# Kernel tuning notes

Hardware: AMD Instinct MI355X
Metric: run time of the kernel (lower is better)

The kernel has to match this reference:

```python
import jax, jax.numpy as jnp
import numpy as np

GRID = (32, 32, 32)
LOWER = jnp.array([0.0, 0.0, 0.0], jnp.float32)
UPPER = jnp.array([1.0, 1.0, 1.0], jnp.float32)
B = 16
N = 131072
C_IN = 1018          # per-point feature channels; +3 offset +3 xyz = 1024 = nn_channels[0]
D_IN = 1024
C_OUT = 128          # nn_channels[-1]
BN_EPS = 1e-5


def setup_inputs() -> dict:
    key = jax.random.key(0)
    ks = jax.random.split(key, 8)
    W1 = jax.random.normal(ks[5], (D_IN, C_OUT), jnp.float32) / np.sqrt(D_IN).astype(np.float32)
    return {
        "xyz": jax.random.uniform(ks[0], (N, 3), jnp.float32),
        "pred_nocs": jax.random.uniform(ks[1], (N, 3), jnp.float32),
        "per_point_features": jax.random.normal(ks[2], (N, C_IN), jnp.float32),
        "pred_confidence": jax.random.uniform(ks[3], (N, 1), jnp.float32),
        "batch_idx": jnp.sort(jax.random.randint(ks[4], (N,), 0, B, dtype=jnp.int32)),
        "batch_size": B,
        "W1": W1,
        "b1": jnp.zeros((C_OUT,), jnp.float32),
        "g1": jnp.ones((C_OUT,), jnp.float32),
        "be1": jnp.zeros((C_OUT,), jnp.float32),
    }


def _batchnorm_train(x, gamma, beta):
    # torch BatchNorm1d in training mode: biased variance over the batch dim
    m = jnp.mean(x, axis=0)
    v = jnp.mean(jnp.square(x - m), axis=0)
    return (x - m) * jax.lax.rsqrt(v + BN_EPS) * gamma + beta


def reference(xyz, pred_nocs, per_point_features, pred_confidence, batch_idx,
              batch_size, W1, b1, g1, be1):
    gs_f = jnp.array(GRID, jnp.float32)
    gs_i = jnp.array(GRID, jnp.int32)
    # VirtualGrid.get_points_grid_idxs: round to nearest cell, clip into grid
    idx_f = jnp.round((pred_nocs - LOWER) / (UPPER - LOWER) * (gs_f - 1.0))
    idx = jnp.clip(idx_f.astype(jnp.int32), 0, gs_i - 1)  # [N,3]
    # VirtualGrid.idxs_to_points
    grid_pts = idx.astype(jnp.float32) / (gs_f - 1.0) * (UPPER - LOWER) + LOWER
    local_offset = pred_nocs - grid_pts
    feats = jnp.concatenate([per_point_features, local_offset, xyz], axis=-1)  # [N,1024]
    # local_nn: Linear -> ReLU -> PointBatchNorm1D
    h = _batchnorm_train(jax.nn.relu(feats @ W1 + b1), g1, be1)  # [N,128]
    # flatten (b,i,j,k) -> flat grid index
    gx, gy, gz = GRID
    flat = ((batch_idx.astype(jnp.int32) * gx + idx[:, 0]) * gy + idx[:, 1]) * gz + idx[:, 2]
    num_grids = batch_size * gx * gy * gz
    ssum = jax.ops.segment_sum(h, flat, num_segments=num_grids)          # [num_grids,128]
    cnt = jax.ops.segment_sum(jnp.ones((h.shape[0], 1), h.dtype), flat, num_segments=num_grids)
    mean = ssum / jnp.maximum(cnt, 1.0)  # empty cells stay 0 (torch_scatter mean)
    # [num_grids, C] -> [B, gx, gy, gz, C] -> [B, C, gx, gy, gz]
    vol = mean.reshape(batch_size, gx, gy, gz, C_OUT).transpose(0, 4, 1, 2, 3)
    return vol
```

## Files before the change

### kernel.cpp

```cpp
#include <hip/hip_runtime.h>

#define NPTS   131072
#define CIN    1018
#define DIN    1024
#define COUT   128
#define BB     16
#define GDIM   32
#define NCELLS (BB*GDIM*GDIM*GDIM)

typedef float          f32x4  __attribute__((ext_vector_type(4)));
typedef __bf16         bf16x8 __attribute__((ext_vector_type(8)));
typedef unsigned short us8    __attribute__((ext_vector_type(8)));

__device__ __forceinline__ unsigned short f2bf(float f) {
    union { float f; unsigned u; } v; v.f = f;
    unsigned r = v.u + 0x7FFFu + ((v.u >> 16) & 1u);
    return (unsigned short)(r >> 16);
}

__global__ __launch_bounds__(256) void k_packW(const float* __restrict__ W1,
                                               unsigned short* __restrict__ pw) {
    const int t  = blockIdx.x * 256 + threadIdx.x;
    const int l  = t & 63;
    const int cb = (t >> 6) & 7;
    const int ks = t >> 9;
    const int col  = cb * 16 + (l & 15);
    const int krow = ks * 32 + ((l >> 4) * 8);
    unsigned short* dst = pw + (size_t)t * 8;
#pragma unroll
    for (int i = 0; i < 8; ++i) dst[i] = f2bf(W1[(size_t)(krow + i) * COUT + col]);
}

__global__ __launch_bounds__(256) void k_prep(const float* __restrict__ xyz,
                                              const float* __restrict__ nocs,
                                              const float* __restrict__ feats,
                                              const int*   __restrict__ bidx,
                                              float* __restrict__ tail,
                                              int*   __restrict__ cellid,
                                              float* __restrict__ count,
                                              float* __restrict__ cellsum,
                                              int zero_cs) {
    const int i = blockIdx.x * 256 + threadIdx.x;
    if (i >= NPTS) return;
    int id[3]; float off[3];
#pragma unroll
    for (int d = 0; d < 3; ++d) {
        const float nv = nocs[i * 3 + d];
        int ii = (int)rintf(nv * 31.0f);
        ii = ii < 0 ? 0 : (ii > 31 ? 31 : ii);
        id[d]  = ii;
        off[d] = nv - (float)ii / 31.0f;
    }
    float* tl = tail + (size_t)i * 8;
    tl[0] = feats[(size_t)i * CIN + 1016];
    tl[1] = feats[(size_t)i * CIN + 1017];
    tl[2] = off[0]; tl[3] = off[1]; tl[4] = off[2];
    tl[5] = xyz[i*3+0]; tl[6] = xyz[i*3+1]; tl[7] = xyz[i*3+2];
    const int cell = ((bidx[i] * GDIM + id[0]) * GDIM + id[1]) * GDIM + id[2];
    cellid[i] = cell;
    unsafeAtomicAdd(count + cell, 1.0f);
    if (zero_cs) {
        f32x4* p = (f32x4*)(cellsum + (size_t)cell * COUT);
        f32x4 z; z[0] = z[1] = z[2] = z[3] = 0.f;
#pragma unroll
        for (int q = 0; q < 32; ++q) p[q] = z;
    }
}

__device__ __forceinline__ us8 cvt8(const float2* v) {
    bf16x8 r;
    r[0] = (__bf16)v[0].x; r[1] = (__bf16)v[0].y;
    r[2] = (__bf16)v[1].x; r[3] = (__bf16)v[1].y;
    r[4] = (__bf16)v[2].x; r[5] = (__bf16)v[2].y;
    r[6] = (__bf16)v[3].x; r[7] = (__bf16)v[3].y;
    return __builtin_bit_cast(us8, r);
}

#define LOADA_FRAG(dst, pr, tl, kg) do{                                  \
    const float* _s = ((kg) == 1016) ? (tl) : ((pr) + (kg));             \
    dst[0] = ((const float2*)_s)[0]; dst[1] = ((const float2*)_s)[1];    \
    dst[2] = ((const float2*)_s)[2]; dst[3] = ((const float2*)_s)[3];    \
}while(0)

#define LOADCHUNK(A00,A01,A10,A11, ch) do{                               \
    const int _k = (ch) * 64 + kgrp * 8;                                 \
    LOADA_FRAG(A00, pr0, tl0, _k);                                       \
    LOADA_FRAG(A01, pr0, tl0, _k + 32);                                  \
    LOADA_FRAG(A10, pr1, tl1, _k);                                       \
    LOADA_FRAG(A11, pr1, tl1, _k + 32);                                  \
}while(0)

#define DOCHUNK(A00,A01,A10,A11, ch) do{                                 \
    us8 b_[2][8];                                                        \
    _Pragma("unroll")                                                    \
    for (int ks = 0; ks < 2; ++ks)                                       \
        _Pragma("unroll")                                                \
        for (int cb = 0; cb < 8; ++cb)                                   \
            b_[ks][cb] = *(const us8*)(pw +                              \
                (((size_t)(ch)*16 + ks*8 + cb)*64 + l)*8);               \
    const us8 a00 = cvt8(A00), a01 = cvt8(A01);                          \
    const us8 a10 = cvt8(A10), a11 = cvt8(A11);                          \
    _Pragma("unroll")                                                    \
    for (int cb = 0; cb < 8; ++cb) {                                     \
        acc0[cb] = __builtin_amdgcn_mfma_f32_16x16x32_bf16(              \
            __builtin_bit_cast(bf16x8, a00), __builtin_bit_cast(bf16x8, b_[0][cb]), acc0[cb], 0,0,0); \
        acc1[cb] = __builtin_amdgcn_mfma_f32_16x16x32_bf16(              \
            __builtin_bit_cast(bf16x8, a10), __builtin_bit_cast(bf16x8, b_[0][cb]), acc1[cb], 0,0,0); \
    }                                                                    \
    _Pragma("unroll")                                                    \
    for (int cb = 0; cb < 8; ++cb) {                                     \
        acc0[cb] = __builtin_amdgcn_mfma_f32_16x16x32_bf16(              \
            __builtin_bit_cast(bf16x8, a01), __builtin_bit_cast(bf16x8, b_[1][cb]), acc0[cb], 0,0,0); \
        acc1[cb] = __builtin_amdgcn_mfma_f32_16x16x32_bf16(              \
            __builtin_bit_cast(bf16x8, a11), __builtin_bit_cast(bf16x8, b_[1][cb]), acc1[cb], 0,0,0); \
    }                                                                    \
}while(0)

template<int DIRECT>
__global__ __launch_bounds__(256, 2) void k_gemm(const float* __restrict__ feats,
                                                 const float* __restrict__ tail,
                                                 const int*   __restrict__ cellid,
                                                 const float* __restrict__ b1,
                                                 const unsigned short* __restrict__ pw,
                                                 float* __restrict__ dst,
                                                 float* __restrict__ gstats) {
    __shared__ float lsum[COUT];
    __shared__ float lsq[COUT];
    const int t = threadIdx.x;
    const int w = t >> 6, l = t & 63;
    const int kgrp = l >> 4, l15 = l & 15;
    const int row0 = blockIdx.x * 128 + w * 32;
    if (t < COUT) { lsum[t] = 0.f; lsq[t] = 0.f; }
    __syncthreads();

    const int r0 = row0 + l15, r1 = r0 + 16;
    const float* pr0 = feats + (size_t)r0 * CIN;
    const float* pr1 = feats + (size_t)r1 * CIN;
    const float* tl0 = tail + (size_t)r0 * 8;
    const float* tl1 = tail + (size_t)r1 * 8;

    f32x4 acc0[8], acc1[8];
#pragma unroll
    for (int cb = 0; cb < 8; ++cb) {
#pragma unroll
        for (int d = 0; d < 4; ++d) { acc0[cb][d] = 0.f; acc1[cb][d] = 0.f; }
    }

    float2 X00[4], X01[4], X10[4], X11[4];
    float2 Y00[4], Y01[4], Y10[4], Y11[4];
    LOADCHUNK(X00, X01, X10, X11, 0);
#pragma unroll
    for (int ch = 0; ch < 16; ch += 2) {
        LOADCHUNK(Y00, Y01, Y10, Y11, ch + 1);
        DOCHUNK(X00, X01, X10, X11, ch);
        if (ch + 2 < 16) LOADCHUNK(X00, X01, X10, X11, ch + 2);
        DOCHUNK(Y00, Y01, Y10, Y11, ch + 1);
    }

    int c0[4], c1[4];
#pragma unroll
    for (int j = 0; j < 4; ++j) {
        const int m = kgrp * 4 + j;
        c0[j] = cellid[row0 + m];
        c1[j] = cellid[row0 + m + 16];
    }
#pragma unroll
    for (int cb = 0; cb < 8; ++cb) {
        const int c = cb * 16 + l15;
        const float bias = b1[c];
        float s = 0.f, q = 0.f;
#pragma unroll
        for (int j = 0; j < 4; ++j) {
            float v0 = acc0[cb][j] + bias; v0 = v0 > 0.f ? v0 : 0.f;
            float v1 = acc1[cb][j] + bias; v1 = v1 > 0.f ? v1 : 0.f;
            if (DIRECT) {
                const int a = c0[j], bce = c1[j];
                unsafeAtomicAdd(dst + (((size_t)((a  >> 15) * COUT + c)) << 15) + (a  & 32767), v0);
                unsafeAtomicAdd(dst + (((size_t)((bce >> 15) * COUT + c)) << 15) + (bce & 32767), v1);
            } else {
                unsafeAtomicAdd(dst + (size_t)c0[j] * COUT + c, v0);
                unsafeAtomicAdd(dst + (size_t)c1[j] * COUT + c, v1);
            }
            s += v0 + v1; q += v0 * v0 + v1 * v1;
        }
        s += __shfl_xor(s, 16); s += __shfl_xor(s, 32);
        q += __shfl_xor(q, 16); q += __shfl_xor(q, 32);
        if (l < 16) { atomicAdd(&lsum[c], s); atomicAdd(&lsq[c], q); }
    }
    __syncthreads();
    if (t < COUT) {
        unsafeAtomicAdd(gstats + t, lsum[t]);
        unsafeAtomicAdd(gstats + COUT + t, lsq[t]);
    }
}

__global__ void k_stats(const float* __restrict__ gstats, const float* __restrict__ g1,
                        const float* __restrict__ be1, float* __restrict__ ss) {
    const int c = threadIdx.x;
    const float invn = 1.0f / (float)NPTS;
    const float mean = gstats[c] * invn;
    float var = gstats[COUT + c] * invn - mean * mean;
    var = var < 0.f ? 0.f : var;
    const float sc = g1[c] * rsqrtf(var + 1e-5f);
    ss[c] = sc;
    ss[COUT + c] = be1[c] - mean * sc;
}

__global__ __launch_bounds__(256) void k_out(const float* __restrict__ cellsum,
                                             const float* __restrict__ count,
                                             const float* __restrict__ ss,
                                             float* __restrict__ out) {
    __shared__ float tile[128 * 128];
    __shared__ float linv[128];
    __shared__ float lss[256];
    const int t  = threadIdx.x;
    const int s0 = blockIdx.x * 128;
    const int b = s0 >> 15, sp0 = s0 & 32767;
    if (t < 128) {
        const float cn = count[s0 + t];
        linv[t] = cn > 0.f ? 1.0f / cn : 0.f;
    } else {
        const int c = t - 128;
        lss[c] = ss[c]; lss[128 + c] = ss[COUT + c];
    }
    const int q = t & 31, r8 = t >> 5;
#pragma unroll
    for (int rep = 0; rep < 16; ++rep) {
        const int j = r8 + rep * 8;
        if (count[s0 + j] > 0.f) {
            const f32x4 v = *(const f32x4*)&cellsum[(size_t)(s0 + j) * COUT + q * 4];
#pragma unroll
            for (int d = 0; d < 4; ++d) {
                const int c = q * 4 + d;
                tile[c * 128 + (j ^ (c & 28))] = v[d];
            }
        }
    }
    __syncthreads();
#pragma unroll
    for (int p = 0; p < 16; ++p) {
        const int c = p * 8 + r8;
        const float sc = lss[c], sh = lss[128 + c];
        const int u = c & 28;
        const f32x4 vv = *(const f32x4*)&tile[c * 128 + ((q * 4) ^ u)];
        f32x4 o;
#pragma unroll
        for (int d = 0; d < 4; ++d) {
            const float inv = linv[q * 4 + d];
            o[d] = inv > 0.f ? vv[d] * inv * sc + sh : 0.f;
        }
        *(f32x4*)&out[(((size_t)(b * COUT + c)) << 15) + sp0 + q * 4] = o;
    }
}

__global__ __launch_bounds__(256) void k_norm_inplace(float* __restrict__ out,
                                                      const float* __restrict__ count,
                                                      const float* __restrict__ ss,
                                                      size_t total) {
    const size_t i = ((size_t)blockIdx.x * 256 + threadIdx.x) * 4;
    if (i >= total) return;
    const int c = (int)((i >> 15) & 127);
    const size_t cellb = ((i >> 22) << 15) | (i & 32767);
    f32x4 v = *(f32x4*)&out[i];
    const f32x4 cn = *(const f32x4*)&count[cellb];
    const float sc = ss[c], sh = ss[COUT + c];
#pragma unroll
    for (int d = 0; d < 4; ++d) v[d] = cn[d] > 0.f ? v[d] / cn[d] * sc + sh : 0.f;
    *(f32x4*)&out[i] = v;
}

extern "C" void kernel_launch(void* const* d_in, const int* in_sizes, int n_in,
                              void* d_out, int out_size, void* d_ws, size_t ws_size,
                              hipStream_t stream) {
    const float* xyz   = (const float*)d_in[0];
    const float* nocs  = (const float*)d_in[1];
    const float* feats = (const float*)d_in[2];
    const int*   bidx  = (const int*)d_in[4];
    const float* W1    = (const float*)d_in[6];
    const float* b1    = (const float*)d_in[7];
    const float* g1    = (const float*)d_in[8];
    const float* be1   = (const float*)d_in[9];
    float* out = (float*)d_out;
    float* ws  = (float*)d_ws;

    const size_t CSF = (size_t)NCELLS * COUT;
    const size_t oA_cs   = 0;
    const size_t oA_cnt  = CSF;
    const size_t oA_st   = oA_cnt + NCELLS;
    const size_t oA_ss   = oA_st + 256;
    const size_t oA_tail = oA_ss + 256;
    const size_t oA_cid  = oA_tail + (size_t)NPTS * 8;
    const size_t oA_pw   = oA_cid + NPTS;
    const size_t needA   = (oA_pw + 65536) * sizeof(float);
    const bool planA = ws_size >= needA;

    const size_t oB_cnt = 0, oB_st = NCELLS, oB_ss = oB_st + 256,
                 oB_tail = oB_ss + 256, oB_cid = oB_tail + (size_t)NPTS * 8,
                 oB_pw = oB_cid + NPTS;

    float* cs  = planA ? ws + oA_cs : nullptr;
    float* cnt = ws + (planA ? oA_cnt : oB_cnt);
    float* st  = ws + (planA ? oA_st : oB_st);
    float* ssb = ws + (planA ? oA_ss : oB_ss);
    float* tl  = ws + (planA ? oA_tail : oB_tail);
    int*   cid = (int*)(ws + (planA ? oA_cid : oB_cid));
    unsigned short* pw = (unsigned short*)(ws + (planA ? oA_pw : oB_pw));

    hipMemsetAsync(cnt, 0, (NCELLS + 256) * sizeof(float), stream);
    if (!planA) hipMemsetAsync(out, 0, (size_t)out_size * sizeof(float), stream);

    k_packW<<<64, 256, 0, stream>>>(W1, pw);
    k_prep<<<NPTS / 256, 256, 0, stream>>>(xyz, nocs, feats, bidx, tl, cid, cnt,
                                           planA ? cs : cnt, planA ? 1 : 0);
    if (planA)
        k_gemm<0><<<NPTS / 128, 256, 0, stream>>>(feats, tl, cid, b1, pw, cs, st);
    else
        k_gemm<1><<<NPTS / 128, 256, 0, stream>>>(feats, tl, cid, b1, pw, out, st);
    k_stats<<<1, 128, 0, stream>>>(st, g1, be1, ssb);
    if (planA)
        k_out<<<NCELLS / 128, 256, 0, stream>>>(cs, cnt, ssb, out);
    else {
        const size_t total = (size_t)out_size;
        k_norm_inplace<<<(unsigned)((total + 1023) / 1024), 256, 0, stream>>>(out, cnt, ssb, total);
    }
    (void)in_sizes; (void)n_in; (void)ws_size; (void)d_in;
}
```

Baseline: 383.5 us.

## Stage A tiles into LDS via direct global-to-LDS loads with double buffering

Replaces per-lane register loads of the fp32 feature rows (float2 granularity, strided by row) with cooperative 16-byte global_load_lds transfers into two XOR-swizzled LDS buffers, then reads MFMA fragments from LDS. The intent is more coalesced global access, so each 64-float row segment is fetched contiguously, and overlap of the next chunk's load with the current chunk's MFMAs. In exchange it uses 64KB of LDS per block, which may limit the two-blocks-per-CU launch bound, and it adds two block barriers per pair of chunks. The swizzle is meant to avoid LDS bank conflicts.

```diff
diff --git a/kernel.cpp b/kernel.cpp
--- a/kernel.cpp
+++ b/kernel.cpp
@@ -16,6 +16,13 @@
     union { float f; unsigned u; } v; v.f = f;
     unsigned r = v.u + 0x7FFFu + ((v.u >> 16) & 1u);
     return (unsigned short)(r >> 16);
+}
+
+__device__ __forceinline__ us8 cvt8f(f32x4 lo, f32x4 hi) {
+    bf16x8 r;
+    r[0] = (__bf16)lo[0]; r[1] = (__bf16)lo[1]; r[2] = (__bf16)lo[2]; r[3] = (__bf16)lo[3];
+    r[4] = (__bf16)hi[0]; r[5] = (__bf16)hi[1]; r[6] = (__bf16)hi[2]; r[7] = (__bf16)hi[3];
+    return __builtin_bit_cast(us8, r);
 }
 
 __global__ __launch_bounds__(256) void k_packW(const float* __restrict__ W1,
@@ -67,53 +74,53 @@
     }
 }
 
-__device__ __forceinline__ us8 cvt8(const float2* v) {
-    bf16x8 r;
-    r[0] = (__bf16)v[0].x; r[1] = (__bf16)v[0].y;
-    r[2] = (__bf16)v[1].x; r[3] = (__bf16)v[1].y;
-    r[4] = (__bf16)v[2].x; r[5] = (__bf16)v[2].y;
-    r[6] = (__bf16)v[3].x; r[7] = (__bf16)v[3].y;
-    return __builtin_bit_cast(us8, r);
-}
-
-#define LOADA_FRAG(dst, pr, tl, kg) do{                                  \
-    const float* _s = ((kg) == 1016) ? (tl) : ((pr) + (kg));             \
-    dst[0] = ((const float2*)_s)[0]; dst[1] = ((const float2*)_s)[1];    \
-    dst[2] = ((const float2*)_s)[2]; dst[3] = ((const float2*)_s)[3];    \
+
+#define STAGE(LDSBUF, ch) do{                                             \
+    const int _k0 = (ch) * 64;                                            \
+    _Pragma("unroll")                                                     \
+    for (int _i = 0; _i < 8; ++_i) {                                      \
+        const int _s   = t + _i * 256;              \
+        const int _row = _s >> 4;                                         \
+        const int _c4  = (_s & 15) ^ (_row & 7);                          \
+        const int _k   = _k0 + _c4 * 4;                                   \
+        const float* _src = (_k < 1016)                                   \
+            ? feats + (size_t)(row0b + _row) * CIN + _k                   \
+            : tail  + (size_t)(row0b + _row) * 8 + (_k - 1016);           \
+        __builtin_amdgcn_global_load_lds(                                 \
+            (const __attribute__((address_space(1))) void*)_src,          \
+            (__attribute__((address_space(3))) void*)&LDSBUF[_s * 4],     \
+            16, 0, 0);                                                    \
+    }                                                                     \
 }while(0)
 
-#define LOADCHUNK(A00,A01,A10,A11, ch) do{                               \
-    const int _k = (ch) * 64 + kgrp * 8;                                 \
-    LOADA_FRAG(A00, pr0, tl0, _k);                                       \
-    LOADA_FRAG(A01, pr0, tl0, _k + 32);                                  \
-    LOADA_FRAG(A10, pr1, tl1, _k);                                       \
-    LOADA_FRAG(A11, pr1, tl1, _k + 32);                                  \
+#define LOADB(B, ch) do{                                                  \
+    _Pragma("unroll")                                                     \
+    for (int _ks = 0; _ks < 2; ++_ks)                                     \
+        _Pragma("unroll")                                                 \
+        for (int _cb = 0; _cb < 8; ++_cb)                                 \
+            B[_ks][_cb] = *(const us8*)(pw +                              \
+                (((size_t)(ch)*16 + _ks*8 + _cb)*64 + l)*8);              \
 }while(0)
 
-#define DOCHUNK(A00,A01,A10,A11, ch) do{                                 \
-    us8 b_[2][8];                                                        \
-    _Pragma("unroll")                                                    \
-    for (int ks = 0; ks < 2; ++ks)                                       \
-        _Pragma("unroll")                                                \
-        for (int cb = 0; cb < 8; ++cb)                                   \
-            b_[ks][cb] = *(const us8*)(pw +                              \
-                (((size_t)(ch)*16 + ks*8 + cb)*64 + l)*8);               \
-    const us8 a00 = cvt8(A00), a01 = cvt8(A01);                          \
-    const us8 a10 = cvt8(A10), a11 = cvt8(A11);                          \
-    _Pragma("unroll")                                                    \
-    for (int cb = 0; cb < 8; ++cb) {                                     \
-        acc0[cb] = __builtin_amdgcn_mfma_f32_16x16x32_bf16(              \
-            __builtin_bit_cast(bf16x8, a00), __builtin_bit_cast(bf16x8, b_[0][cb]), acc0[cb], 0,0,0); \
-        acc1[cb] = __builtin_amdgcn_mfma_f32_16x16x32_bf16(              \
-            __builtin_bit_cast(bf16x8, a10), __builtin_bit_cast(bf16x8, b_[0][cb]), acc1[cb], 0,0,0); \
-    }                                                                    \
-    _Pragma("unroll")                                                    \
-    for (int cb = 0; cb < 8; ++cb) {                                     \
-        acc0[cb] = __builtin_amdgcn_mfma_f32_16x16x32_bf16(              \
-            __builtin_bit_cast(bf16x8, a01), __builtin_bit_cast(bf16x8, b_[1][cb]), acc0[cb], 0,0,0); \
-        acc1[cb] = __builtin_amdgcn_mfma_f32_16x16x32_bf16(              \
-            __builtin_bit_cast(bf16x8, a11), __builtin_bit_cast(bf16x8, b_[1][cb]), acc1[cb], 0,0,0); \
-    }                                                                    \
+#define COMPUTE(LDSBUF, B) do{                                            \
+    _Pragma("unroll")                                                     \
+    for (int _ks = 0; _ks < 2; ++_ks) {                                   \
+        const int _c4a = _ks*8 + kgrp*2;                                  \
+        const int _sw  = l15 & 7;                     \
+        const f32x4 _lo0 = *(const f32x4*)&LDSBUF[(lr0*16 + ( _c4a    ^ _sw))*4]; \
+        const f32x4 _hi0 = *(const f32x4*)&LDSBUF[(lr0*16 + ((_c4a+1) ^ _sw))*4]; \
+        const f32x4 _lo1 = *(const f32x4*)&LDSBUF[(lr1*16 + ( _c4a    ^ _sw))*4]; \
+        const f32x4 _hi1 = *(const f32x4*)&LDSBUF[(lr1*16 + ((_c4a+1) ^ _sw))*4]; \
+        const us8 _a0 = cvt8f(_lo0, _hi0);                                \
+        const us8 _a1 = cvt8f(_lo1, _hi1);                                \
+        _Pragma("unroll")                                                 \
+        for (int _cb = 0; _cb < 8; ++_cb) {                               \
+            acc0[_cb] = __builtin_amdgcn_mfma_f32_16x16x32_bf16(          \
+                __builtin_bit_cast(bf16x8,_a0), __builtin_bit_cast(bf16x8,B[_ks][_cb]), acc0[_cb],0,0,0); \
+            acc1[_cb] = __builtin_amdgcn_mfma_f32_16x16x32_bf16(          \
+                __builtin_bit_cast(bf16x8,_a1), __builtin_bit_cast(bf16x8,B[_ks][_cb]), acc1[_cb],0,0,0); \
+        }                                                                 \
+    }                                                                     \
 }while(0)
 
 template<int DIRECT>
@@ -124,37 +131,36 @@
                                                  const unsigned short* __restrict__ pw,
                                                  float* __restrict__ dst,
                                                  float* __restrict__ gstats) {
+    __shared__ float Alds0[128 * 64];
+    __shared__ float Alds1[128 * 64];
     __shared__ float lsum[COUT];
     __shared__ float lsq[COUT];
     const int t = threadIdx.x;
     const int w = t >> 6, l = t & 63;
     const int kgrp = l >> 4, l15 = l & 15;
-    const int row0 = blockIdx.x * 128 + w * 32;
+    const int row0b = blockIdx.x * 128;
+    const int row0 = row0b + w * 32;
     if (t < COUT) { lsum[t] = 0.f; lsq[t] = 0.f; }
+
+    const int lr0 = w * 32 + l15, lr1 = lr0 + 16;
+
+    f32x4 acc0[8], acc1[8];
+#pragma unroll
+    for (int cb = 0; cb < 8; ++cb) {
+#pragma unroll
+        for (int d = 0; d < 4; ++d) { acc0[cb][d] = 0.f; acc1[cb][d] = 0.f; }
+    }
+
+    us8 BX[2][8], BY[2][8];
+    STAGE(Alds0, 0); LOADB(BX, 0);
     __syncthreads();
-
-    const int r0 = row0 + l15, r1 = r0 + 16;
-    const float* pr0 = feats + (size_t)r0 * CIN;
-    const float* pr1 = feats + (size_t)r1 * CIN;
-    const float* tl0 = tail + (size_t)r0 * 8;
-    const float* tl1 = tail + (size_t)r1 * 8;
-
-    f32x4 acc0[8], acc1[8];
-#pragma unroll
-    for (int cb = 0; cb < 8; ++cb) {
-#pragma unroll
-        for (int d = 0; d < 4; ++d) { acc0[cb][d] = 0.f; acc1[cb][d] = 0.f; }
-    }
-
-    float2 X00[4], X01[4], X10[4], X11[4];
-    float2 Y00[4], Y01[4], Y10[4], Y11[4];
-    LOADCHUNK(X00, X01, X10, X11, 0);
-#pragma unroll
     for (int ch = 0; ch < 16; ch += 2) {
-        LOADCHUNK(Y00, Y01, Y10, Y11, ch + 1);
-        DOCHUNK(X00, X01, X10, X11, ch);
-        if (ch + 2 < 16) LOADCHUNK(X00, X01, X10, X11, ch + 2);
-        DOCHUNK(Y00, Y01, Y10, Y11, ch + 1);
+        STAGE(Alds1, ch + 1); LOADB(BY, ch + 1);
+        COMPUTE(Alds0, BX);
+        __syncthreads();
+        if (ch + 2 < 16) { STAGE(Alds0, ch + 2); LOADB(BX, ch + 2); }
+        COMPUTE(Alds1, BY);
+        __syncthreads();
     }
 
     int c0[4], c1[4];
```

New measurement: 452.6 us. 1.18x slower.
